# Optimization experiments

Measured on AMD Instinct MI355X. Metric: run time of the kernel, lower is better.

## Reference

```python
import jax, jax.numpy as jnp
import numpy as np

N = 50000        # nodes
E = 600000       # edges (no self-loops; reference adds N self-loops)
IN_C = 64
OUT_C = 64
HEADS = 2
NEG_SLOPE = 0.2  # GraphLayer default negative_slope
BN_EPS = 1e-5


def setup_inputs() -> dict:
    key = jax.random.key(0)
    ks = jax.random.split(key, 14)
    x = jax.random.normal(ks[0], (N, IN_C), dtype=jnp.float32)
    # edge_index with no self-loops by construction (original calls remove_self_loops)
    src = jax.random.randint(ks[1], (E,), 0, N, dtype=jnp.int32)
    off = jax.random.randint(ks[2], (E,), 1, N, dtype=jnp.int32)
    dst = (src + off) % N
    edge_index = jnp.stack([src, dst])  # [2, E]
    embedding = jax.random.normal(ks[3], (N, OUT_C), dtype=jnp.float32)
    s = 0.1
    lin_w = jax.random.normal(ks[4], (IN_C, HEADS * OUT_C), dtype=jnp.float32) * s
    att_i = jax.random.normal(ks[5], (1, HEADS, OUT_C), dtype=jnp.float32) * s
    att_j = jax.random.normal(ks[6], (1, HEADS, OUT_C), dtype=jnp.float32) * s
    att_em_i = jax.random.normal(ks[7], (1, HEADS, OUT_C), dtype=jnp.float32) * s
    att_em_j = jax.random.normal(ks[8], (1, HEADS, OUT_C), dtype=jnp.float32) * s
    gnn_bias = jnp.zeros((HEADS * OUT_C,), dtype=jnp.float32)
    ff_w = jax.random.normal(ks[9], (HEADS * OUT_C, OUT_C), dtype=jnp.float32) * s
    ff_b = jnp.zeros((OUT_C,), dtype=jnp.float32)
    bn_gamma = jnp.ones((OUT_C,), dtype=jnp.float32)
    bn_beta = jnp.zeros((OUT_C,), dtype=jnp.float32)
    return {"x": x, "edge_index": edge_index, "embedding": embedding,
            "lin_w": lin_w, "att_i": att_i, "att_j": att_j,
            "att_em_i": att_em_i, "att_em_j": att_em_j, "gnn_bias": gnn_bias,
            "ff_w": ff_w, "ff_b": ff_b, "bn_gamma": bn_gamma, "bn_beta": bn_beta}


def reference(x, edge_index, embedding, lin_w, att_i, att_j, att_em_i, att_em_j,
              gnn_bias, ff_w, ff_b, bn_gamma, bn_beta):
    n = x.shape[0]
    h = (x @ lin_w).reshape(n, HEADS, OUT_C)  # lin projection, per-head view
    # add self-loops (input already has none)
    ar = jnp.arange(n, dtype=edge_index.dtype)
    ei = jnp.concatenate([edge_index, jnp.stack([ar, ar])], axis=1)
    src, dst = ei[0], ei[1]                   # x_j = source, x_i = target
    x_i, x_j = h[dst], h[src]                 # [Et, H, C]
    emb_i = embedding[dst][:, None, :]        # [Et, 1, C] broadcast over heads
    emb_j = embedding[src][:, None, :]
    # alpha = <cat(x_i,emb_i), cat(att_i,att_em_i)> + <cat(x_j,emb_j), cat(att_j,att_em_j)>
    alpha = ((x_i * att_i[0]).sum(-1) + (emb_i * att_em_i[0]).sum(-1)
             + (x_j * att_j[0]).sum(-1) + (emb_j * att_em_j[0]).sum(-1))  # [Et, H]
    alpha = jax.nn.leaky_relu(alpha, NEG_SLOPE)
    # segment softmax over incoming edges of each target node (PyG softmax)
    amax = jax.ops.segment_max(alpha, dst, num_segments=n)
    ex = jnp.exp(alpha - amax[dst])
    denom = jax.ops.segment_sum(ex, dst, num_segments=n)
    alpha = ex / (denom[dst] + 1e-16)
    out = jax.ops.segment_sum(x_j * alpha[:, :, None], dst, num_segments=n)  # [n,H,C]
    out = out.reshape(n, HEADS * OUT_C) + gnn_bias  # concat heads + bias
    out = out @ ff_w + ff_b                         # self.ff
    mean = out.mean(axis=0)                          # BatchNorm1d, training stats
    var = out.var(axis=0)                            # biased variance (torch BN)
    out = (out - mean) / jnp.sqrt(var + BN_EPS) * bn_gamma + bn_beta
    return jax.nn.relu(out)
```

## Files before the change

### kernel.cpp

```cpp
#include <hip/hip_runtime.h>

#define C 64
#define HC 128
#define NEG 0.2f

typedef __attribute__((ext_vector_type(8))) short bf16x8;
typedef __attribute__((ext_vector_type(4))) float f32x4;

__device__ __forceinline__ float lrelu(float v) { return v >= 0.f ? v : NEG * v; }
__device__ __forceinline__ unsigned short f2bf(float f) {
    unsigned u = __float_as_uint(f);
    return (unsigned short)((u + 0x7fffu + ((u >> 16) & 1u)) >> 16);
}
__device__ __forceinline__ float bflo(unsigned u) { return __uint_as_float(u << 16); }
__device__ __forceinline__ float bfhi(unsigned u) { return __uint_as_float(u & 0xffff0000u); }

__global__ __launch_bounds__(256) void kA_mfma_edge(
    const float* __restrict__ x, const float* __restrict__ lin_w,
    const float* __restrict__ emb,
    const float* __restrict__ att_i, const float* __restrict__ att_j,
    const float* __restrict__ att_em_i, const float* __restrict__ att_em_j,
    unsigned* __restrict__ hb, float2* __restrict__ a_i2,
    float2* __restrict__ a_j2, int n_nodes, int nb64,
    const int* __restrict__ dstv, int* __restrict__ deg,
    int* __restrict__ rank, int e)
{
    const int t = threadIdx.x;
    if (blockIdx.x >= nb64) {
        const int i = (blockIdx.x - nb64) * 256 + t;
        if (i < e) rank[i] = atomicAdd(&deg[dstv[i]], 1);
        return;
    }
    __shared__ __align__(16) char smem[8192];
    const int lane = t & 63, w = t >> 6;
    const int r = lane & 15, g = lane >> 4;

    bf16x8 B[4][2][2];
#pragma unroll
    for (int m4 = 0; m4 < 4; ++m4)
#pragma unroll
        for (int p = 0; p < 2; ++p)
#pragma unroll
            for (int kk = 0; kk < 2; ++kk) {
                bf16x8 bb;
#pragma unroll
                for (int j = 0; j < 8; ++j)
                    bb[j] = (short)f2bf(lin_w[(kk * 32 + 8 * g + j) * HC + 32 * m4 + 2 * r + p]);
                B[m4][p][kk] = bb;
            }
    float wi[4][2], wj[4][2];
#pragma unroll
    for (int m4 = 0; m4 < 4; ++m4)
#pragma unroll
        for (int p = 0; p < 2; ++p) {
            wi[m4][p] = att_i[32 * m4 + 2 * r + p];
            wj[m4][p] = att_j[32 * m4 + 2 * r + p];
        }
    float wem_i0[4], wem_i1[4], wem_j0[4], wem_j1[4];
#pragma unroll
    for (int q = 0; q < 4; ++q) {
        wem_i0[q] = att_em_i[q * 16 + r];
        wem_i1[q] = att_em_i[64 + q * 16 + r];
        wem_j0[q] = att_em_j[q * 16 + r];
        wem_j1[q] = att_em_j[64 + q * 16 + r];
    }

    {
        const int row = t >> 2, q = t & 3;
        const int gn = blockIdx.x * 64 + row;
        float ff[16];
        if (gn < n_nodes) {
            const float4* xs = (const float4*)(x + (size_t)gn * C + q * 16);
            *(float4*)&ff[0] = xs[0]; *(float4*)&ff[4] = xs[1];
            *(float4*)&ff[8] = xs[2]; *(float4*)&ff[12] = xs[3];
        } else {
#pragma unroll
            for (int j = 0; j < 16; ++j) ff[j] = 0.f;
        }
        bf16x8 p0, p1;
#pragma unroll
        for (int j = 0; j < 8; ++j) {
            p0[j] = (short)f2bf(ff[j]);
            p1[j] = (short)f2bf(ff[8 + j]);
        }
        const unsigned bb = (unsigned)((row >> 4) * 2048 + (row & 15) * 128 + q * 32);
        const unsigned sw = (unsigned)((row & 7) << 4);
        *(bf16x8*)(smem + ((bb) ^ sw)) = p0;
        *(bf16x8*)(smem + ((bb + 16) ^ sw)) = p1;
    }
    __syncthreads();

    bf16x8 A[2];
    const unsigned ab = (unsigned)(w * 2048 + r * 128 + g * 16);
    const unsigned sw = (unsigned)((r & 7) << 4);
    A[0] = *(const bf16x8*)(smem + ((ab) ^ sw));
    A[1] = *(const bf16x8*)(smem + ((ab + 64) ^ sw));

    f32x4 acc[4][2];
#pragma unroll
    for (int m4 = 0; m4 < 4; ++m4)
#pragma unroll
        for (int p = 0; p < 2; ++p) acc[m4][p] = (f32x4){0.f, 0.f, 0.f, 0.f};
#pragma unroll
    for (int kk = 0; kk < 2; ++kk)
#pragma unroll
        for (int m4 = 0; m4 < 4; ++m4)
#pragma unroll
            for (int p = 0; p < 2; ++p)
                acc[m4][p] = __builtin_amdgcn_mfma_f32_16x16x32_bf16(A[kk], B[m4][p][kk], acc[m4][p], 0, 0, 0);

    const int nb = blockIdx.x * 64 + w * 16 + 4 * g;
#pragma unroll
    for (int j = 0; j < 4; ++j) {
        const int rr = nb + j;
        if (rr < n_nodes) {
            float pi0 = 0.f, pi1 = 0.f, pj0 = 0.f, pj1 = 0.f;
            unsigned* hp = hb + (size_t)rr * 64 + r;
#pragma unroll
            for (int m4 = 0; m4 < 4; ++m4) {
                const float ev = acc[m4][0][j], ov = acc[m4][1][j];
                hp[m4 * 16] = ((unsigned)f2bf(ov) << 16) | (unsigned)f2bf(ev);
                if (m4 < 2) {
                    pi0 = fmaf(ev, wi[m4][0], fmaf(ov, wi[m4][1], pi0));
                    pj0 = fmaf(ev, wj[m4][0], fmaf(ov, wj[m4][1], pj0));
                } else {
                    pi1 = fmaf(ev, wi[m4][0], fmaf(ov, wi[m4][1], pi1));
                    pj1 = fmaf(ev, wj[m4][0], fmaf(ov, wj[m4][1], pj1));
                }
            }
#pragma unroll
            for (int q = 0; q < 4; ++q) {
                const float ev = emb[(size_t)rr * C + q * 16 + r];
                pi0 = fmaf(ev, wem_i0[q], pi0);
                pi1 = fmaf(ev, wem_i1[q], pi1);
                pj0 = fmaf(ev, wem_j0[q], pj0);
                pj1 = fmaf(ev, wem_j1[q], pj1);
            }
#pragma unroll
            for (int m = 1; m < 16; m <<= 1) {
                pi0 += __shfl_xor(pi0, m, 64);
                pi1 += __shfl_xor(pi1, m, 64);
                pj0 += __shfl_xor(pj0, m, 64);
                pj1 += __shfl_xor(pj1, m, 64);
            }
            if (r == 0) {
                a_i2[rr] = make_float2(pi0, pi1);
                a_j2[rr] = make_float2(pj0, pj1);
            }
        }
    }
}

__global__ __launch_bounds__(256) void k_scan(
    const int* __restrict__ deg, int* __restrict__ counter,
    int* __restrict__ rowptr, int n)
{
    __shared__ int sh[256];
    __shared__ int s_base;
    const int t = threadIdx.x;
    const int i0 = blockIdx.x * 512 + t * 2;
    const int a = (i0 < n) ? deg[i0] : 0;
    const int b = (i0 + 1 < n) ? deg[i0 + 1] : 0;
    const int s = a + b;
    sh[t] = s;
    __syncthreads();
    for (int off = 1; off < 256; off <<= 1) {
        int v = (t >= off) ? sh[t - off] : 0;
        __syncthreads();
        sh[t] += v;
        __syncthreads();
    }
    const int excl = sh[t] - s;
    if (t == 255) s_base = atomicAdd(counter, sh[255]);
    __syncthreads();
    const int base = s_base;
    if (i0 < n)     rowptr[i0]     = base + excl;
    if (i0 + 1 < n) rowptr[i0 + 1] = base + excl + a;
}

__global__ __launch_bounds__(256) void k_fill(
    const int* __restrict__ srcv, const int* __restrict__ dstv,
    const int* __restrict__ rank, const int* __restrict__ rowptr,
    int* __restrict__ csr, int e)
{
    int i = blockIdx.x * 256 + threadIdx.x;
    if (i >= e) return;
    csr[rowptr[dstv[i]] + rank[i]] = srcv[i];
}

__global__ __launch_bounds__(256) void kD_gff(
    const int* __restrict__ csr, const int* __restrict__ rowptr,
    const int* __restrict__ deg, const unsigned* __restrict__ hb,
    const float2* __restrict__ a_i2, const float2* __restrict__ a_j2,
    const float2* __restrict__ bias2, const float* __restrict__ ff_w,
    const float* __restrict__ ff_b, float* __restrict__ out2,
    float* __restrict__ partial, int n_nodes)
{
    __shared__ __align__(16) char smem[4096];
    const int t = threadIdx.x;
    const int lane = t & 63, w = t >> 6;
    const int r = lane & 15, g = lane >> 4;

    bf16x8 B[4];
#pragma unroll
    for (int kk = 0; kk < 4; ++kk) {
        bf16x8 bb;
#pragma unroll
        for (int j = 0; j < 8; ++j)
            bb[j] = (short)f2bf(ff_w[(kk * 32 + 8 * g + j) * C + w * 16 + r]);
        B[kk] = bb;
    }
    const float fb = ff_b[w * 16 + r];
    const float2 bv = bias2[lane];

    const int nbase = blockIdx.x * 16;
#pragma unroll
    for (int j = 0; j < 4; ++j) {
        const int n = nbase + w * 4 + j;
        unsigned packed = 0;
        if (n < n_nodes) {
            const int r0 = __builtin_amdgcn_readfirstlane(rowptr[n]);
            const int r1 = r0 + __builtin_amdgcn_readfirstlane(deg[n]);
            const float2 ai = a_i2[n];
            const float2 ajs = a_j2[n];
            const float es0 = __expf(lrelu(ai.x + ajs.x));
            const float es1 = __expf(lrelu(ai.y + ajs.y));
            float den0 = es0, den1 = es1;
            const unsigned hv = hb[(size_t)n * 64 + lane];
            const float exs = (lane < 32) ? es0 : es1;
            float2 acc = make_float2(exs * bflo(hv), exs * bfhi(hv));
#pragma unroll 4
            for (int rr = r0; rr < r1; ++rr) {
                const int se = csr[rr];
                const float2 aj = a_j2[se];
                const float ex0 = __expf(lrelu(ai.x + aj.x));
                const float ex1 = __expf(lrelu(ai.y + aj.y));
                den0 += ex0; den1 += ex1;
                const float exh = (lane < 32) ? ex0 : ex1;
                const unsigned v = hb[(size_t)se * 64 + lane];
                acc.x = fmaf(exh, bflo(v), acc.x);
                acc.y = fmaf(exh, bfhi(v), acc.y);
            }
            const float den = (lane < 32) ? den0 : den1;
            const float inv = 1.f / (den + 1e-16f);
            packed = ((unsigned)f2bf(fmaf(acc.y, inv, bv.y)) << 16)
                   | (unsigned)f2bf(fmaf(acc.x, inv, bv.x));
        }
        const int row = w * 4 + j;
        const unsigned byte = (unsigned)(row * 256 + lane * 4);
        *(unsigned*)(smem + (byte ^ ((unsigned)(row & 7) << 4))) = packed;
    }
    __syncthreads();

    bf16x8 A[4];
#pragma unroll
    for (int kk = 0; kk < 4; ++kk) {
        const unsigned byte = (unsigned)(r * 256 + kk * 64 + g * 16);
        A[kk] = *(const bf16x8*)(smem + (byte ^ ((unsigned)(r & 7) << 4)));
    }
    f32x4 acc4 = (f32x4){0.f, 0.f, 0.f, 0.f};
#pragma unroll
    for (int kk = 0; kk < 4; ++kk)
        acc4 = __builtin_amdgcn_mfma_f32_16x16x32_bf16(A[kk], B[kk], acc4, 0, 0, 0);

    float st = 0.f, st2 = 0.f;
#pragma unroll
    for (int jj = 0; jj < 4; ++jj) {
        const int rr = nbase + 4 * g + jj;
        if (rr < n_nodes) {
            const float v = acc4[jj] + fb;
            out2[(size_t)rr * C + w * 16 + r] = v;
            st += v; st2 = fmaf(v, v, st2);
        }
    }
    st  += __shfl_xor(st, 16, 64);  st  += __shfl_xor(st, 32, 64);
    st2 += __shfl_xor(st2, 16, 64); st2 += __shfl_xor(st2, 32, 64);
    if (g == 0) {
        partial[(size_t)blockIdx.x * 128 + w * 16 + r] = st;
        partial[(size_t)blockIdx.x * 128 + 64 + w * 16 + r] = st2;
    }
}

__global__ __launch_bounds__(256) void k5_red(
    const float* __restrict__ partial, float* __restrict__ colsum,
    float* __restrict__ colsq, int nblk)
{
    __shared__ float sh[256];
    const int c = blockIdx.x;
    const int t = threadIdx.x;
    float s = 0.f;
    for (int b = t; b < nblk; b += 256) s += partial[(size_t)b * 128 + c];
    sh[t] = s;
    __syncthreads();
    for (int off = 128; off; off >>= 1) {
        if (t < off) sh[t] += sh[t + off];
        __syncthreads();
    }
    if (t == 0) {
        if (c < C) colsum[c] = sh[0];
        else       colsq[c - C] = sh[0];
    }
}

__global__ __launch_bounds__(256) void k6_bn(
    float* __restrict__ out2, const float* __restrict__ colsum,
    const float* __restrict__ colsq, const float* __restrict__ gamma,
    const float* __restrict__ beta, float inv_n, int total )
{
    int i = blockIdx.x * 256 + threadIdx.x;
    if (i >= total) return;
    int c = i & 63;
    float mean = colsum[c] * inv_n;
    float var = colsq[c] * inv_n - mean * mean;
    float rstd = rsqrtf(var + 1e-5f);
    float v = (out2[i] - mean) * rstd * gamma[c] + beta[c];
    out2[i] = fmaxf(v, 0.f);
}

extern "C" void kernel_launch(void* const* d_in, const int* in_sizes, int n_in,
                              void* d_out, int out_size, void* d_ws, size_t ws_size,
                              hipStream_t stream)
{
    const float* x        = (const float*)d_in[0];
    const int*   ei       = (const int*)d_in[1];
    const float* emb      = (const float*)d_in[2];
    const float* lin_w    = (const float*)d_in[3];
    const float* att_i    = (const float*)d_in[4];
    const float* att_j    = (const float*)d_in[5];
    const float* att_em_i = (const float*)d_in[6];
    const float* att_em_j = (const float*)d_in[7];
    const float* gnn_bias = (const float*)d_in[8];
    const float* ff_w     = (const float*)d_in[9];
    const float* ff_b     = (const float*)d_in[10];
    const float* bn_g     = (const float*)d_in[11];
    const float* bn_b     = (const float*)d_in[12];

    const int n = in_sizes[0] / C;
    const int e = in_sizes[1] / 2;
    const int* srcv = ei;
    const int* dstv = ei + e;

    const int nb64  = (n + 63) / 64;
    const int nb16  = (n + 15) / 16;
    const int nbE   = (e + 255) / 256;

    float* ws = (float*)d_ws;
    unsigned* hb      = (unsigned*)ws;
    float*    a_if    = (float*)(hb + (size_t)n * 64);
    float*    a_jf    = a_if + 2 * (size_t)n;
    float*    partial = a_jf + 2 * (size_t)n;
    float*    colsum  = partial + (size_t)nb16 * 128;
    float*    colsq   = colsum + C;
    int*      deg     = (int*)(colsq + C);
    int*      counter = deg + n;
    int*      rowptr  = counter + 1;
    int*      rank    = rowptr + n;
    int*      csr     = rank + e;
    float*    out2    = (float*)d_out;

    hipMemsetAsync(deg, 0, (size_t)(n + 1) * sizeof(int), stream);

    kA_mfma_edge<<<nb64 + nbE, 256, 0, stream>>>(
        x, lin_w, emb, att_i, att_j, att_em_i, att_em_j,
        hb, (float2*)a_if, (float2*)a_jf, n, nb64, dstv, deg, rank, e);
    k_scan<<<(n + 511) / 512, 256, 0, stream>>>(deg, counter, rowptr, n);
    k_fill<<<nbE, 256, 0, stream>>>(srcv, dstv, rank, rowptr, csr, e);
    kD_gff<<<nb16, 256, 0, stream>>>(csr, rowptr, deg, hb,
                                     (const float2*)a_if, (const float2*)a_jf,
                                     (const float2*)gnn_bias, ff_w, ff_b,
                                     out2, partial, n);
    k5_red<<<128, 256, 0, stream>>>(partial, colsum, colsq, nb16);
    {
        int total = n * C;
        k6_bn<<<(total + 255) / 256, 256, 0, stream>>>(out2, colsum, colsq, bn_g, bn_b,
                                                       1.0f / (float)n, total);
    }
}
```

Before: 201.9 us.

## Precompute edge softmax weights in CSR fill and pre-pack bf16 weight fragments

The CSR fill kernel now computes each edge's leaky-relu attention exponent for both heads and stores it as packed fp16 next to the source index. The aggregation loop then reads one int2 per edge instead of doing a dependent gather of a_j plus two exps. A new prep kernel converts lin_w and ff_w into bf16 MFMA fragment layout once and zeroes the degree counters, which replaces the memset and the per-block strided weight conversion. The cost is a wider CSR array, an extra launch, and exp values held at fp16 precision without max-subtraction, which can overflow or lose precision for large logits.

```diff
diff --git a/kernel.cpp b/kernel.cpp
--- a/kernel.cpp
+++ b/kernel.cpp
@@ -6,6 +6,7 @@
 
 typedef __attribute__((ext_vector_type(8))) short bf16x8;
 typedef __attribute__((ext_vector_type(4))) float f32x4;
+typedef __fp16 fp16x2 __attribute__((ext_vector_type(2)));
 
 __device__ __forceinline__ float lrelu(float v) { return v >= 0.f ? v : NEG * v; }
 __device__ __forceinline__ unsigned short f2bf(float f) {
@@ -15,8 +16,37 @@
 __device__ __forceinline__ float bflo(unsigned u) { return __uint_as_float(u << 16); }
 __device__ __forceinline__ float bfhi(unsigned u) { return __uint_as_float(u & 0xffff0000u); }
 
+__global__ __launch_bounds__(256) void k_prep(
+    const float* __restrict__ lin_w, const float* __restrict__ ff_w,
+    bf16x8* __restrict__ linb, bf16x8* __restrict__ ffb,
+    int* __restrict__ deg_counter, int nz)
+{
+    const int i = blockIdx.x * 256 + threadIdx.x;
+    if (i < nz) deg_counter[i] = 0;
+    if (i < 1024) {
+        const int lane = i & 63, frag = i >> 6;
+        const int r = lane & 15, g = lane >> 4;
+        const int m4 = frag >> 2, p = (frag >> 1) & 1, kk = frag & 1;
+        bf16x8 bb;
+#pragma unroll
+        for (int j = 0; j < 8; ++j)
+            bb[j] = (short)f2bf(lin_w[(kk * 32 + 8 * g + j) * HC + 32 * m4 + 2 * r + p]);
+        linb[i] = bb;
+    } else if (i < 2048) {
+        const int i2 = i - 1024;
+        const int lane = i2 & 63, frag = i2 >> 6;
+        const int r = lane & 15, g = lane >> 4;
+        const int w = frag >> 2, kk = frag & 3;
+        bf16x8 bb;
+#pragma unroll
+        for (int j = 0; j < 8; ++j)
+            bb[j] = (short)f2bf(ff_w[(kk * 32 + 8 * g + j) * C + w * 16 + r]);
+        ffb[i2] = bb;
+    }
+}
+
 __global__ __launch_bounds__(256) void kA_mfma_edge(
-    const float* __restrict__ x, const float* __restrict__ lin_w,
+    const float* __restrict__ x, const bf16x8* __restrict__ linb,
     const float* __restrict__ emb,
     const float* __restrict__ att_i, const float* __restrict__ att_j,
     const float* __restrict__ att_em_i, const float* __restrict__ att_em_j,
@@ -41,13 +71,9 @@
 #pragma unroll
         for (int p = 0; p < 2; ++p)
 #pragma unroll
-            for (int kk = 0; kk < 2; ++kk) {
-                bf16x8 bb;
-#pragma unroll
-                for (int j = 0; j < 8; ++j)
-                    bb[j] = (short)f2bf(lin_w[(kk * 32 + 8 * g + j) * HC + 32 * m4 + 2 * r + p]);
-                B[m4][p][kk] = bb;
-            }
+            for (int kk = 0; kk < 2; ++kk)
+                B[m4][p][kk] = linb[(m4 * 4 + p * 2 + kk) * 64 + lane];
+
     float wi[4][2], wj[4][2];
 #pragma unroll
     for (int m4 = 0; m4 < 4; ++m4)
@@ -181,18 +207,26 @@
 __global__ __launch_bounds__(256) void k_fill(
     const int* __restrict__ srcv, const int* __restrict__ dstv,
     const int* __restrict__ rank, const int* __restrict__ rowptr,
-    int* __restrict__ csr, int e)
+    const float2* __restrict__ a_i2, const float2* __restrict__ a_j2,
+    int2* __restrict__ edata, int e)
 {
     int i = blockIdx.x * 256 + threadIdx.x;
     if (i >= e) return;
-    csr[rowptr[dstv[i]] + rank[i]] = srcv[i];
+    const int s = srcv[i], d = dstv[i];
+    const float2 ai = a_i2[d];
+    const float2 aj = a_j2[s];
+    const float ex0 = __expf(lrelu(ai.x + aj.x));
+    const float ex1 = __expf(lrelu(ai.y + aj.y));
+    union { fp16x2 h; int u; } cv;
+    cv.h = __builtin_amdgcn_cvt_pkrtz(ex0, ex1);
+    edata[rowptr[d] + rank[i]] = make_int2(s, cv.u);
 }
 
 __global__ __launch_bounds__(256) void kD_gff(
-    const int* __restrict__ csr, const int* __restrict__ rowptr,
+    const int2* __restrict__ edata, const int* __restrict__ rowptr,
     const int* __restrict__ deg, const unsigned* __restrict__ hb,
     const float2* __restrict__ a_i2, const float2* __restrict__ a_j2,
-    const float2* __restrict__ bias2, const float* __restrict__ ff_w,
+    const float2* __restrict__ bias2, const bf16x8* __restrict__ ffb,
     const float* __restrict__ ff_b, float* __restrict__ out2,
     float* __restrict__ partial, int n_nodes)
 {
@@ -203,13 +237,7 @@
 
     bf16x8 B[4];
 #pragma unroll
-    for (int kk = 0; kk < 4; ++kk) {
-        bf16x8 bb;
-#pragma unroll
-        for (int j = 0; j < 8; ++j)
-            bb[j] = (short)f2bf(ff_w[(kk * 32 + 8 * g + j) * C + w * 16 + r]);
-        B[kk] = bb;
-    }
+    for (int kk = 0; kk < 4; ++kk) B[kk] = ffb[(w * 4 + kk) * 64 + lane];
     const float fb = ff_b[w * 16 + r];
     const float2 bv = bias2[lane];
 
@@ -231,10 +259,11 @@
             float2 acc = make_float2(exs * bflo(hv), exs * bfhi(hv));
 #pragma unroll 4
             for (int rr = r0; rr < r1; ++rr) {
-                const int se = csr[rr];
-                const float2 aj = a_j2[se];
-                const float ex0 = __expf(lrelu(ai.x + aj.x));
-                const float ex1 = __expf(lrelu(ai.y + aj.y));
+                const int2 ed = edata[rr];
+                const int se = ed.x;
+                union { int u; fp16x2 h; } cv; cv.u = ed.y;
+                const float ex0 = (float)cv.h[0];
+                const float ex1 = (float)cv.h[1];
                 den0 += ex0; den1 += ex1;
                 const float exh = (lane < 32) ? ex0 : ex1;
                 const unsigned v = hb[(size_t)se * 64 + lane];
@@ -340,34 +369,38 @@
     const int* srcv = ei;
     const int* dstv = ei + e;
 
-    const int nb64  = (n + 63) / 64;
-    const int nb16  = (n + 15) / 16;
-    const int nbE   = (e + 255) / 256;
+    const int nb64 = (n + 63) / 64;
+    const int nb16 = (n + 15) / 16;
+    const int nbE  = (e + 255) / 256;
 
     float* ws = (float*)d_ws;
     unsigned* hb      = (unsigned*)ws;
-    float*    a_if    = (float*)(hb + (size_t)n * 64);
+    bf16x8*   linb    = (bf16x8*)(hb + (size_t)n * 64);
+    bf16x8*   ffb     = linb + 1024;
+    float*    a_if    = (float*)(ffb + 1024);
     float*    a_jf    = a_if + 2 * (size_t)n;
     float*    partial = a_jf + 2 * (size_t)n;
     float*    colsum  = partial + (size_t)nb16 * 128;
     float*    colsq   = colsum + C;
     int*      deg     = (int*)(colsq + C);
     int*      counter = deg + n;
-    int*      rowptr  = counter + 1;
+    int*      rowptr  = counter + 2;
     int*      rank    = rowptr + n;
-    int*      csr     = rank + e;
+    int2*     edata   = (int2*)(rank + e);
     float*    out2    = (float*)d_out;
 
-    hipMemsetAsync(deg, 0, (size_t)(n + 1) * sizeof(int), stream);
-
+    k_prep<<<(n + 2 + 255) / 256, 256, 0, stream>>>(lin_w, ff_w, linb, ffb,
+                                                    deg, n + 2);
     kA_mfma_edge<<<nb64 + nbE, 256, 0, stream>>>(
-        x, lin_w, emb, att_i, att_j, att_em_i, att_em_j,
+        x, linb, emb, att_i, att_j, att_em_i, att_em_j,
         hb, (float2*)a_if, (float2*)a_jf, n, nb64, dstv, deg, rank, e);
     k_scan<<<(n + 511) / 512, 256, 0, stream>>>(deg, counter, rowptr, n);
-    k_fill<<<nbE, 256, 0, stream>>>(srcv, dstv, rank, rowptr, csr, e);
-    kD_gff<<<nb16, 256, 0, stream>>>(csr, rowptr, deg, hb,
+    k_fill<<<nbE, 256, 0, stream>>>(srcv, dstv, rank, rowptr,
+                                    (const float2*)a_if, (const float2*)a_jf,
+                                    edata, e);
+    kD_gff<<<nb16, 256, 0, stream>>>(edata, rowptr, deg, hb,
                                      (const float2*)a_if, (const float2*)a_jf,
-                                     (const float2*)gnn_bias, ff_w, ff_b,
+                                     (const float2*)gnn_bias, ffb, ff_b,
                                      out2, partial, n);
     k5_red<<<128, 256, 0, stream>>>(partial, colsum, colsq, nb16);
     {
```

After: 190.7 us. 5.5% less time.
